# Performance work log

Measured on AMD Instinct MI355X. Metric: run time of the kernel, lower is better.

## Reference

```python
import jax, jax.numpy as jnp
import numpy as np

N = 65536      # nodes (256x256 grid)
E = 1048576    # edges (avg degree 16)
T_IN = 10      # TIME_STEPS_IN
L = 64         # LATENT_DIMS
MID = 128      # LATENT_DIMS * MLP_RATIO
GD = 2         # grid dims


def _lin_init(key, fan_in, fan_out):
    kw, kb = jax.random.split(key)
    s = 1.0 / np.sqrt(fan_in)
    W = jax.random.uniform(kw, (fan_in, fan_out), jnp.float32, -s, s)
    b = jax.random.uniform(kb, (fan_out,), jnp.float32, -s, s)
    return W, b


def setup_inputs() -> dict:
    key = jax.random.key(0)
    ks = jax.random.split(key, 10)
    x = jax.random.normal(ks[0], (N, T_IN), jnp.float32)
    grid = jax.random.uniform(ks[1], (N, GD), jnp.float32)
    edge_index = jax.random.randint(ks[2], (2, E), 0, N, jnp.int64)
    W_proj1, b_proj1 = _lin_init(ks[3], T_IN + GD, MID)
    W_proj2, b_proj2 = _lin_init(ks[4], MID, L)
    Wk, bk = _lin_init(ks[5], 2 * L + 2 * GD + 1, L)   # K edge MLP (single linear)
    Ww, bw = _lin_init(ks[6], L, L)                     # W node MLP (single linear)
    W_dec1, b_dec1 = _lin_init(ks[7], L, MID)
    W_dec2, b_dec2 = _lin_init(ks[8], MID, 1)
    return {"x": x, "grid": grid, "edge_index": edge_index,
            "W_proj1": W_proj1, "b_proj1": b_proj1, "W_proj2": W_proj2, "b_proj2": b_proj2,
            "Wk": Wk, "bk": bk, "Ww": Ww, "bw": bw,
            "W_dec1": W_dec1, "b_dec1": b_dec1, "W_dec2": W_dec2, "b_dec2": b_dec2}


def _gelu(x):
    return jax.nn.gelu(x, approximate=False)  # torch F.gelu default = exact erf


def reference(x, grid, edge_index, W_proj1, b_proj1, W_proj2, b_proj2,
              Wk, bk, Ww, bw, W_dec1, b_dec1, W_dec2, b_dec2):
    # project: cat(x, grid) -> Linear -> GELU -> Linear
    h = jnp.concatenate([x, grid], axis=-1)               # [N, T_IN+2]
    h = _gelu(h @ W_proj1 + b_proj1) @ W_proj2 + b_proj2  # [N, L]

    # message passing block (PyG source_to_target: j = row 0, i = row 1)
    src = edge_index[0]
    dst = edge_index[1]
    x_j = h[src]                                          # [E, L]
    x_i = h[dst]                                          # [E, L]
    g_j = grid[src]                                       # [E, 2]
    g_i = grid[dst]                                       # [E, 2]
    dist = jnp.sqrt(jnp.sum(jnp.square(g_i - g_j), axis=-1, keepdims=True))  # [E, 1]
    ef = jnp.concatenate([dist, g_i, g_j, x_i, x_j], axis=-1)  # [E, 2L+5]
    msg = ef @ Wk + bk                                    # [E, L]
    aggr = jax.ops.segment_sum(msg, dst, num_segments=N)  # [N, L]
    h = _gelu(h @ Ww + bw + aggr)                         # update

    # decode: Linear -> GELU -> Linear
    out = _gelu(h @ W_dec1 + b_dec1) @ W_dec2 + b_dec2    # [N, 1]
    return out
```

## Files before the change

kernel.cpp:

```cpp
#include <hip/hip_runtime.h>
#include <hip/hip_fp16.h>

static __device__ __forceinline__ float gelu(float x) {
    return 0.5f * x * (1.0f + erff(x * 0.70710678118654752f));
}

#define NBE 64
#define CAP 64

typedef _Float16 v8h __attribute__((ext_vector_type(8)));
typedef float    v4f __attribute__((ext_vector_type(4)));
union F8 { uint4 u; v8h v; _Float16 f[8]; };

static __device__ __forceinline__ void acc8(float* a, uint4 u) {
    float2 f0 = __half22float2(*(__half2*)&u.x);
    float2 f1 = __half22float2(*(__half2*)&u.y);
    float2 f2 = __half22float2(*(__half2*)&u.z);
    float2 f3 = __half22float2(*(__half2*)&u.w);
    a[0] += f0.x; a[1] += f0.y; a[2] += f1.x; a[3] += f1.y;
    a[4] += f2.x; a[5] += f2.y; a[6] += f3.x; a[7] += f3.y;
}

static __device__ __forceinline__ uint4 pack8(const float* v) {
    __half2 p0 = __floats2half2_rn(v[0], v[1]);
    __half2 p1 = __floats2half2_rn(v[2], v[3]);
    __half2 p2 = __floats2half2_rn(v[4], v[5]);
    __half2 p3 = __floats2half2_rn(v[6], v[7]);
    uint4 u;
    u.x = *(unsigned*)&p0; u.y = *(unsigned*)&p1;
    u.z = *(unsigned*)&p2; u.w = *(unsigned*)&p3;
    return u;
}

__global__ void __launch_bounds__(256, 1)
k_enc_scat(const float* __restrict__ x,
           const float* __restrict__ grid,
           const float* __restrict__ W1,
           const float* __restrict__ b1,
           const float* __restrict__ W2,
           const float* __restrict__ b2,
           const int* __restrict__ ei, int* __restrict__ cnt,
           int* __restrict__ ssrc,
           __half* __restrict__ h16, int N, int E, int encB)
{
    __shared__ float sx[NBE * 10];
    __shared__ float sg[NBE * 2];
    __shared__ float sm[NBE * 132];
    int tid = threadIdx.x;
    if ((int)blockIdx.x >= encB) {
        int e4 = (blockIdx.x - encB) * 256 + tid;
        if (e4 * 4 < E) {
            const int4* s4 = (const int4*)ei;
            const int4* d4 = (const int4*)(ei + E);
            int4 s = s4[e4];
            int4 d = d4[e4];
            int p;
            p = atomicAdd(&cnt[d.x], 1); if (p < CAP) ssrc[((size_t)d.x << 6) + p] = s.x;
            p = atomicAdd(&cnt[d.y], 1); if (p < CAP) ssrc[((size_t)d.y << 6) + p] = s.y;
            p = atomicAdd(&cnt[d.z], 1); if (p < CAP) ssrc[((size_t)d.z << 6) + p] = s.z;
            p = atomicAdd(&cnt[d.w], 1); if (p < CAP) ssrc[((size_t)d.w << 6) + p] = s.w;
        }
        return;
    }
    int n0 = blockIdx.x * NBE;
    for (int i = tid; i < NBE * 10; i += 256) sx[i] = x[(size_t)n0 * 10 + i];
    if (tid < NBE * 2) sg[tid] = grid[(size_t)n0 * 2 + tid];
    __syncthreads();

    int l = tid & 7, r = tid >> 3;
    int mb = 16 * l;
    float in[2][12];
#pragma unroll
    for (int m = 0; m < 2; m++) {
        int node = r + 32 * m;
#pragma unroll
        for (int k = 0; k < 10; k++) in[m][k] = sx[node * 10 + k];
        in[m][10] = sg[node * 2 + 0];
        in[m][11] = sg[node * 2 + 1];
    }

    float macc[2][16];
#pragma unroll
    for (int i = 0; i < 16; i++) {
        float b = b1[mb + i];
        macc[0][i] = b; macc[1][i] = b;
    }
#pragma unroll
    for (int k = 0; k < 12; k++) {
        const float4* w = (const float4*)(W1 + k * 128 + mb);
#pragma unroll
        for (int q = 0; q < 4; q++) {
            float4 wv = w[q];
#pragma unroll
            for (int m = 0; m < 2; m++) {
                float xv = in[m][k];
                macc[m][4 * q + 0] += xv * wv.x;
                macc[m][4 * q + 1] += xv * wv.y;
                macc[m][4 * q + 2] += xv * wv.z;
                macc[m][4 * q + 3] += xv * wv.w;
            }
        }
    }
#pragma unroll
    for (int m = 0; m < 2; m++) {
        float4* smp = (float4*)(sm + (r + 32 * m) * 132 + mb);
#pragma unroll
        for (int q = 0; q < 4; q++)
            smp[q] = make_float4(gelu(macc[m][4 * q]), gelu(macc[m][4 * q + 1]),
                                 gelu(macc[m][4 * q + 2]), gelu(macc[m][4 * q + 3]));
    }
    __syncthreads();

    int ob = 8 * l;
    float out8[2][8];
#pragma unroll
    for (int j = 0; j < 8; j++) {
        float b = b2[ob + j];
        out8[0][j] = b; out8[1][j] = b;
    }
#pragma unroll 2
    for (int i4 = 0; i4 < 128; i4 += 4) {
        float mva[2][4];
#pragma unroll
        for (int m = 0; m < 2; m++)
            *(float4*)mva[m] = *(const float4*)&sm[(r + 32 * m) * 132 + i4];
#pragma unroll
        for (int ii = 0; ii < 4; ii++) {
            const float4* w = (const float4*)(W2 + (i4 + ii) * 64 + ob);
            float4 w0 = w[0], w1 = w[1];
#pragma unroll
            for (int m = 0; m < 2; m++) {
                float mv = mva[m][ii];
                out8[m][0] += mv * w0.x; out8[m][1] += mv * w0.y;
                out8[m][2] += mv * w0.z; out8[m][3] += mv * w0.w;
                out8[m][4] += mv * w1.x; out8[m][5] += mv * w1.y;
                out8[m][6] += mv * w1.z; out8[m][7] += mv * w1.w;
            }
        }
    }
#pragma unroll
    for (int m = 0; m < 2; m++)
        ((uint4*)(h16 + (size_t)(n0 + r + 32 * m) * 64))[l] = pack8(out8[m]);
}

__global__ void k_gather(const __half* __restrict__ h16,
                         const float* __restrict__ grid,
                         const int* __restrict__ ssrc, const int* __restrict__ cnt,
                         __half* __restrict__ sum_h16, float* __restrict__ sum_g,
                         float* __restrict__ sum_d, int N)
{
    int tid = blockIdx.x * blockDim.x + threadIdx.x;
    int n = tid >> 3;
    int l = tid & 7;
    if (n >= N) return;
    int beg = n << 6;
    int dg = min(cnt[n], CAP);
    const uint4* h8 = (const uint4*)h16;
    float a0[8] = {0,0,0,0,0,0,0,0};
    float a1[8] = {0,0,0,0,0,0,0,0};
    float a2[8] = {0,0,0,0,0,0,0,0};
    float a3[8] = {0,0,0,0,0,0,0,0};
    float sgx = 0.f, sgy = 0.f, sd = 0.f, gix = 0.f, giy = 0.f;
    if (l == 0) { gix = grid[2 * n]; giy = grid[2 * n + 1]; }
    int i = 0;
    for (; i + 3 < dg; i += 4) {
        int4 s = *(const int4*)&ssrc[beg + i];
        uint4 u0 = h8[(size_t)s.x * 8 + l];
        uint4 u1 = h8[(size_t)s.y * 8 + l];
        uint4 u2 = h8[(size_t)s.z * 8 + l];
        uint4 u3 = h8[(size_t)s.w * 8 + l];
        acc8(a0, u0); acc8(a1, u1); acc8(a2, u2); acc8(a3, u3);
        if (l == 0) {
            float gx0 = grid[2 * s.x], gy0 = grid[2 * s.x + 1];
            float gx1 = grid[2 * s.y], gy1 = grid[2 * s.y + 1];
            float gx2 = grid[2 * s.z], gy2 = grid[2 * s.z + 1];
            float gx3 = grid[2 * s.w], gy3 = grid[2 * s.w + 1];
            float dx0 = gix - gx0, dy0 = giy - gy0;
            float dx1 = gix - gx1, dy1 = giy - gy1;
            float dx2 = gix - gx2, dy2 = giy - gy2;
            float dx3 = gix - gx3, dy3 = giy - gy3;
            sd += sqrtf(dx0 * dx0 + dy0 * dy0) + sqrtf(dx1 * dx1 + dy1 * dy1)
                + sqrtf(dx2 * dx2 + dy2 * dy2) + sqrtf(dx3 * dx3 + dy3 * dy3);
            sgx += gx0 + gx1 + gx2 + gx3;
            sgy += gy0 + gy1 + gy2 + gy3;
        }
    }
    for (; i < dg; i++) {
        int s0 = ssrc[beg + i];
        uint4 u0 = h8[(size_t)s0 * 8 + l];
        acc8(a0, u0);
        if (l == 0) {
            float gx0 = grid[2 * s0], gy0 = grid[2 * s0 + 1];
            float dx0 = gix - gx0, dy0 = giy - gy0;
            sd += sqrtf(dx0 * dx0 + dy0 * dy0);
            sgx += gx0; sgy += gy0;
        }
    }
#pragma unroll
    for (int j = 0; j < 8; j++) a0[j] += a1[j] + a2[j] + a3[j];
    ((uint4*)(sum_h16 + (size_t)n * 64))[l] = pack8(a0);
    if (l == 0) { sum_d[n] = sd; sum_g[2 * n] = sgx; sum_g[2 * n + 1] = sgy; }
}

__global__ void __launch_bounds__(256, 1)
k_update(const __half* __restrict__ h16, __half* __restrict__ sum_h16,
         const float* __restrict__ sum_g, const float* __restrict__ sum_d,
         const int* __restrict__ cnt, const float* __restrict__ grid,
         const float* __restrict__ Wk, const float* __restrict__ bk,
         const float* __restrict__ Ww, const float* __restrict__ bw, int N)
{
    __shared__ uint4 tabW[512];
    __shared__ uint4 tabC[512];
    __shared__ uint4 tabD[512];
    __shared__ uint4 tabV[256];
    int tid = threadIdx.x;

    for (int idx = tid; idx < 512; idx += 256) {
        int lane = idx & 63, nt = (idx >> 6) & 3, kc = idx >> 8;
        int col = nt * 16 + (lane & 15);
        int kr  = kc * 32 + ((lane >> 4) << 3);
        F8 fw, fc, fd;
#pragma unroll
        for (int j = 0; j < 8; j++) {
            fw.f[j] = (_Float16)Ww[(kr + j) * 64 + col];
            fc.f[j] = (_Float16)Wk[(size_t)(5 + kr + j) * 64 + col];
            fd.f[j] = (_Float16)Wk[(size_t)(69 + kr + j) * 64 + col];
        }
        tabW[idx] = fw.u; tabC[idx] = fc.u; tabD[idx] = fd.u;
    }
    if (tid < 256) {
        int lane = tid & 63, nt = tid >> 6;
        int col = nt * 16 + (lane & 15);
        F8 fv;
#pragma unroll
        for (int j = 0; j < 8; j++) fv.f[j] = (_Float16)0.f;
        if ((lane >> 4) == 0) {
            fv.f[0] = (_Float16)bw[col];
            fv.f[1] = (_Float16)bk[col];
            fv.f[2] = (_Float16)Wk[col];
            fv.f[3] = (_Float16)Wk[64 + col];
            fv.f[4] = (_Float16)Wk[128 + col];
            fv.f[5] = (_Float16)Wk[192 + col];
            fv.f[6] = (_Float16)Wk[256 + col];
        }
        tabV[tid] = fv.u;
    }
    __syncthreads();

    int lane = tid & 63, wave = tid >> 6;
    int m = lane & 15, quad = lane >> 4;
    const uint4* h8 = (const uint4*)h16;
    const uint4* s8 = (const uint4*)sum_h16;

    for (int t = 0; t < 2; t++) {
        int tile = blockIdx.x * 8 + wave * 2 + t;
        int base = tile * 16;
        int n = base + m;
        float deg = (float)cnt[n];
        float sd  = sum_d[n];
        float sgx = sum_g[2 * n], sgy = sum_g[2 * n + 1];
        float gix = grid[2 * n] * deg, giy = grid[2 * n + 1] * deg;

        F8 ah0, ah1, as0, as1, ahd0, ahd1, au;
        ah0.u = h8[(size_t)n * 8 + quad];
        ah1.u = h8[(size_t)n * 8 + 4 + quad];
        as0.u = s8[(size_t)n * 8 + quad];
        as1.u = s8[(size_t)n * 8 + 4 + quad];
        _Float16 dh = (_Float16)deg;
#pragma unroll
        for (int j = 0; j < 8; j++) { ahd0.f[j] = ah0.f[j] * dh; ahd1.f[j] = ah1.f[j] * dh; }
        float z = (quad == 0) ? 1.f : 0.f;
        au.f[0] = (_Float16)z;          au.f[1] = (_Float16)(deg * z);
        au.f[2] = (_Float16)(sd * z);   au.f[3] = (_Float16)(gix * z);
        au.f[4] = (_Float16)(giy * z);  au.f[5] = (_Float16)(sgx * z);
        au.f[6] = (_Float16)(sgy * z);  au.f[7] = (_Float16)0.f;

        float h2v[4][4];
#pragma unroll
        for (int nt = 0; nt < 4; nt++) {
            F8 bv, bw0, bw1, bc0, bc1, bd0, bd1f;
            bv.u  = tabV[nt * 64 + lane];
            bw0.u = tabW[nt * 64 + lane];       bw1.u = tabW[256 + nt * 64 + lane];
            bc0.u = tabC[nt * 64 + lane];       bc1.u = tabC[256 + nt * 64 + lane];
            bd0.u = tabD[nt * 64 + lane];       bd1f.u = tabD[256 + nt * 64 + lane];
            v4f acc = {0.f, 0.f, 0.f, 0.f};
            acc = __builtin_amdgcn_mfma_f32_16x16x32_f16(au.v,   bv.v,   acc, 0, 0, 0);
            acc = __builtin_amdgcn_mfma_f32_16x16x32_f16(ah0.v,  bw0.v,  acc, 0, 0, 0);
            acc = __builtin_amdgcn_mfma_f32_16x16x32_f16(ah1.v,  bw1.v,  acc, 0, 0, 0);
            acc = __builtin_amdgcn_mfma_f32_16x16x32_f16(ahd0.v, bc0.v,  acc, 0, 0, 0);
            acc = __builtin_amdgcn_mfma_f32_16x16x32_f16(ahd1.v, bc1.v,  acc, 0, 0, 0);
            acc = __builtin_amdgcn_mfma_f32_16x16x32_f16(as0.v,  bd0.v,  acc, 0, 0, 0);
            acc = __builtin_amdgcn_mfma_f32_16x16x32_f16(as1.v,  bd1f.v, acc, 0, 0, 0);
#pragma unroll
            for (int reg = 0; reg < 4; reg++) h2v[nt][reg] = gelu(acc[reg]);
        }
#pragma unroll
        for (int reg = 0; reg < 4; reg++) {
            int nr = base + quad * 4 + reg;
#pragma unroll
            for (int nt = 0; nt < 4; nt++)
                sum_h16[(size_t)nr * 64 + m + 16 * nt] = __float2half(h2v[nt][reg]);
        }
    }
}

__global__ void __launch_bounds__(256, 1)
k_decode(const __half* __restrict__ h2g,
         const float* __restrict__ Wd1, const float* __restrict__ bd1,
         const float* __restrict__ Wd2, const float* __restrict__ bd2,
         float* __restrict__ out, int N)
{
    __shared__ uint4 tab[1024];
    int tid = threadIdx.x;
    for (int idx = tid; idx < 1024; idx += 256) {
        int lane = idx & 63, nt = (idx >> 6) & 7, kc = idx >> 9;
        int col = nt * 16 + (lane & 15);
        int kr  = kc * 32 + ((lane >> 4) << 3);
        F8 f;
#pragma unroll
        for (int j = 0; j < 8; j++) f.f[j] = (_Float16)Wd1[(kr + j) * 128 + col];
        tab[idx] = f.u;
    }
    __syncthreads();

    int lane = tid & 63, wave = tid >> 6;
    int m = lane & 15, quad = lane >> 4;
    const uint4* h8 = (const uint4*)h2g;
    float bd2v = bd2[0];

    for (int t = 0; t < 2; t++) {
        int tile = blockIdx.x * 8 + wave * 2 + t;
        int base = tile * 16;
        int n = base + m;
        F8 ah0, ah1;
        ah0.u = h8[(size_t)n * 8 + quad];
        ah1.u = h8[(size_t)n * 8 + 4 + quad];
        float p[4] = {0.f, 0.f, 0.f, 0.f};
#pragma unroll
        for (int nt = 0; nt < 8; nt++) {
            int col = m + 16 * nt;
            float b = bd1[col];
            float w2 = Wd2[col];
            F8 b0, b1;
            b0.u = tab[nt * 64 + lane];
            b1.u = tab[512 + nt * 64 + lane];
            v4f acc = {b, b, b, b};
            acc = __builtin_amdgcn_mfma_f32_16x16x32_f16(ah0.v, b0.v, acc, 0, 0, 0);
            acc = __builtin_amdgcn_mfma_f32_16x16x32_f16(ah1.v, b1.v, acc, 0, 0, 0);
#pragma unroll
            for (int reg = 0; reg < 4; reg++) p[reg] += gelu(acc[reg]) * w2;
        }
#pragma unroll
        for (int reg = 0; reg < 4; reg++) {
            p[reg] += __shfl_xor(p[reg], 1);
            p[reg] += __shfl_xor(p[reg], 2);
            p[reg] += __shfl_xor(p[reg], 4);
            p[reg] += __shfl_xor(p[reg], 8);
        }
        if (m == 0) {
#pragma unroll
            for (int reg = 0; reg < 4; reg++)
                out[base + quad * 4 + reg] = p[reg] + bd2v;
        }
    }
}

extern "C" void kernel_launch(void* const* d_in, const int* in_sizes, int n_in,
                              void* d_out, int out_size, void* d_ws, size_t ws_size,
                              hipStream_t stream)
{
    const float* x    = (const float*)d_in[0];
    const float* grid = (const float*)d_in[1];
    const int*   ei   = (const int*)d_in[2];
    const float* W1   = (const float*)d_in[3];
    const float* b1   = (const float*)d_in[4];
    const float* W2   = (const float*)d_in[5];
    const float* b2   = (const float*)d_in[6];
    const float* Wk   = (const float*)d_in[7];
    const float* bk   = (const float*)d_in[8];
    const float* Ww   = (const float*)d_in[9];
    const float* bw   = (const float*)d_in[10];
    const float* Wd1  = (const float*)d_in[11];
    const float* bd1  = (const float*)d_in[12];
    const float* Wd2  = (const float*)d_in[13];
    const float* bd2  = (const float*)d_in[14];
    float* out = (float*)d_out;

    int N = in_sizes[0] / 10;
    int E = in_sizes[2] / 2;

    char* ws = (char*)d_ws;
    size_t o_h16  = 0;
    size_t o_sh16 = o_h16  + (size_t)N * 64 * 2;
    size_t o_sumg = o_sh16 + (size_t)N * 64 * 2;
    size_t o_sumd = o_sumg + (size_t)N * 2 * 4;
    size_t o_cnt  = o_sumd + (size_t)N * 4;
    size_t o_ssrc = o_cnt  + (size_t)N * 4;

    __half* h16     = (__half*)(ws + o_h16);
    __half* sum_h16 = (__half*)(ws + o_sh16);
    float* sum_g = (float*)(ws + o_sumg);
    float* sum_d = (float*)(ws + o_sumd);
    int*   cnt   = (int*)  (ws + o_cnt);
    int*   ssrc  = (int*)  (ws + o_ssrc);

    hipMemsetAsync(cnt, 0, (size_t)N * 4, stream);

    int encB  = N / NBE;
    int scatB = (E / 4 + 255) / 256;
    k_enc_scat<<<dim3(encB + scatB), dim3(256), 0, stream>>>(x, grid, W1, b1, W2, b2,
                                                             ei, cnt, ssrc, h16, N, E, encB);
    k_gather<<<dim3((N * 8 + 255) / 256), dim3(256), 0, stream>>>(h16, grid, ssrc, cnt,
                                                                   sum_h16, sum_g, sum_d, N);
    int tiles = N / 16;
    k_update<<<dim3(tiles / 8), dim3(256), 0, stream>>>(h16, sum_h16, sum_g, sum_d, cnt,
                                                        grid, Wk, bk, Ww, bw, N);
    k_decode<<<dim3(tiles / 8), dim3(256), 0, stream>>>(sum_h16, Wd1, bd1, Wd2, bd2, out, N);
}
```

Baseline: 235.4 us.

## Store edge source indices as 16-bit, parallelize grid gather, shrink encoder tile

Edge source indices in the CSR-like bucket are stored as unsigned short, which halves the scatter writes and the gather index reads. The gather kernel spreads the per-edge grid loads and distance math across four lanes and combines them with xor shuffles instead of serializing on lane 0. The encoder now processes 32 nodes per block and keeps the hidden activations in fp16 shared memory, with one node per thread group. The 16-bit indices only hold for N up to 65536, and the fp16 intermediate adds rounding.

After: 284.1 us. +20.7%, slower.

```diff
diff --git a/kernel.cpp b/kernel.cpp
--- a/kernel.cpp
+++ b/kernel.cpp
@@ -5,7 +5,8 @@
     return 0.5f * x * (1.0f + erff(x * 0.70710678118654752f));
 }
 
-#define NBE 64
+#define NBE 32
+#define SM  136
 #define CAP 64
 
 typedef _Float16 v8h __attribute__((ext_vector_type(8)));
@@ -40,12 +41,12 @@
            const float* __restrict__ W2,
            const float* __restrict__ b2,
            const int* __restrict__ ei, int* __restrict__ cnt,
-           int* __restrict__ ssrc,
+           unsigned short* __restrict__ ssrc,
            __half* __restrict__ h16, int N, int E, int encB)
 {
     __shared__ float sx[NBE * 10];
     __shared__ float sg[NBE * 2];
-    __shared__ float sm[NBE * 132];
+    __shared__ __half sm[NBE * SM];
     int tid = threadIdx.x;
     if ((int)blockIdx.x >= encB) {
         int e4 = (blockIdx.x - encB) * 256 + tid;
@@ -55,10 +56,10 @@
             int4 s = s4[e4];
             int4 d = d4[e4];
             int p;
-            p = atomicAdd(&cnt[d.x], 1); if (p < CAP) ssrc[((size_t)d.x << 6) + p] = s.x;
-            p = atomicAdd(&cnt[d.y], 1); if (p < CAP) ssrc[((size_t)d.y << 6) + p] = s.y;
-            p = atomicAdd(&cnt[d.z], 1); if (p < CAP) ssrc[((size_t)d.z << 6) + p] = s.z;
-            p = atomicAdd(&cnt[d.w], 1); if (p < CAP) ssrc[((size_t)d.w << 6) + p] = s.w;
+            p = atomicAdd(&cnt[d.x], 1); if (p < CAP) ssrc[((size_t)d.x << 6) + p] = (unsigned short)s.x;
+            p = atomicAdd(&cnt[d.y], 1); if (p < CAP) ssrc[((size_t)d.y << 6) + p] = (unsigned short)s.y;
+            p = atomicAdd(&cnt[d.z], 1); if (p < CAP) ssrc[((size_t)d.z << 6) + p] = (unsigned short)s.z;
+            p = atomicAdd(&cnt[d.w], 1); if (p < CAP) ssrc[((size_t)d.w << 6) + p] = (unsigned short)s.w;
         }
         return;
     }
@@ -67,85 +68,71 @@
     if (tid < NBE * 2) sg[tid] = grid[(size_t)n0 * 2 + tid];
     __syncthreads();
 
-    int l = tid & 7, r = tid >> 3;
+    int l = tid & 7, nl = tid >> 3;
     int mb = 16 * l;
-    float in[2][12];
-#pragma unroll
-    for (int m = 0; m < 2; m++) {
-        int node = r + 32 * m;
-#pragma unroll
-        for (int k = 0; k < 10; k++) in[m][k] = sx[node * 10 + k];
-        in[m][10] = sg[node * 2 + 0];
-        in[m][11] = sg[node * 2 + 1];
-    }
-
-    float macc[2][16];
-#pragma unroll
-    for (int i = 0; i < 16; i++) {
-        float b = b1[mb + i];
-        macc[0][i] = b; macc[1][i] = b;
-    }
+    float in[12];
+#pragma unroll
+    for (int k = 0; k < 10; k++) in[k] = sx[nl * 10 + k];
+    in[10] = sg[nl * 2 + 0];
+    in[11] = sg[nl * 2 + 1];
+
+    float macc[16];
+#pragma unroll
+    for (int i = 0; i < 16; i++) macc[i] = b1[mb + i];
 #pragma unroll
     for (int k = 0; k < 12; k++) {
+        float xv = in[k];
         const float4* w = (const float4*)(W1 + k * 128 + mb);
 #pragma unroll
         for (int q = 0; q < 4; q++) {
             float4 wv = w[q];
-#pragma unroll
-            for (int m = 0; m < 2; m++) {
-                float xv = in[m][k];
-                macc[m][4 * q + 0] += xv * wv.x;
-                macc[m][4 * q + 1] += xv * wv.y;
-                macc[m][4 * q + 2] += xv * wv.z;
-                macc[m][4 * q + 3] += xv * wv.w;
-            }
-        }
-    }
-#pragma unroll
-    for (int m = 0; m < 2; m++) {
-        float4* smp = (float4*)(sm + (r + 32 * m) * 132 + mb);
-#pragma unroll
-        for (int q = 0; q < 4; q++)
-            smp[q] = make_float4(gelu(macc[m][4 * q]), gelu(macc[m][4 * q + 1]),
-                                 gelu(macc[m][4 * q + 2]), gelu(macc[m][4 * q + 3]));
-    }
+            macc[4 * q + 0] += xv * wv.x;
+            macc[4 * q + 1] += xv * wv.y;
+            macc[4 * q + 2] += xv * wv.z;
+            macc[4 * q + 3] += xv * wv.w;
+        }
+    }
+    float g16[16];
+#pragma unroll
+    for (int i = 0; i < 16; i++) g16[i] = gelu(macc[i]);
+    *(uint4*)&sm[nl * SM + mb]     = pack8(g16);
+    *(uint4*)&sm[nl * SM + mb + 8] = pack8(g16 + 8);
     __syncthreads();
 
     int ob = 8 * l;
-    float out8[2][8];
-#pragma unroll
-    for (int j = 0; j < 8; j++) {
-        float b = b2[ob + j];
-        out8[0][j] = b; out8[1][j] = b;
-    }
+    float out8[8];
+#pragma unroll
+    for (int j = 0; j < 8; j++) out8[j] = b2[ob + j];
+    const __half* smn = sm + nl * SM;
 #pragma unroll 2
-    for (int i4 = 0; i4 < 128; i4 += 4) {
-        float mva[2][4];
-#pragma unroll
-        for (int m = 0; m < 2; m++)
-            *(float4*)mva[m] = *(const float4*)&sm[(r + 32 * m) * 132 + i4];
-#pragma unroll
-        for (int ii = 0; ii < 4; ii++) {
-            const float4* w = (const float4*)(W2 + (i4 + ii) * 64 + ob);
+    for (int i8 = 0; i8 < 128; i8 += 8) {
+        F8 mu;
+        mu.u = *(const uint4*)&smn[i8];
+        float mv[8];
+        float2 t0 = __half22float2(*(__half2*)&mu.u.x);
+        float2 t1 = __half22float2(*(__half2*)&mu.u.y);
+        float2 t2 = __half22float2(*(__half2*)&mu.u.z);
+        float2 t3 = __half22float2(*(__half2*)&mu.u.w);
+        mv[0] = t0.x; mv[1] = t0.y; mv[2] = t1.x; mv[3] = t1.y;
+        mv[4] = t2.x; mv[5] = t2.y; mv[6] = t3.x; mv[7] = t3.y;
+#pragma unroll
+        for (int ii = 0; ii < 8; ii++) {
+            const float4* w = (const float4*)(W2 + (i8 + ii) * 64 + ob);
             float4 w0 = w[0], w1 = w[1];
-#pragma unroll
-            for (int m = 0; m < 2; m++) {
-                float mv = mva[m][ii];
-                out8[m][0] += mv * w0.x; out8[m][1] += mv * w0.y;
-                out8[m][2] += mv * w0.z; out8[m][3] += mv * w0.w;
-                out8[m][4] += mv * w1.x; out8[m][5] += mv * w1.y;
-                out8[m][6] += mv * w1.z; out8[m][7] += mv * w1.w;
-            }
-        }
-    }
-#pragma unroll
-    for (int m = 0; m < 2; m++)
-        ((uint4*)(h16 + (size_t)(n0 + r + 32 * m) * 64))[l] = pack8(out8[m]);
+            float m = mv[ii];
+            out8[0] += m * w0.x; out8[1] += m * w0.y;
+            out8[2] += m * w0.z; out8[3] += m * w0.w;
+            out8[4] += m * w1.x; out8[5] += m * w1.y;
+            out8[6] += m * w1.z; out8[7] += m * w1.w;
+        }
+    }
+    ((uint4*)(h16 + (size_t)(n0 + nl) * 64))[l] = pack8(out8);
 }
 
 __global__ void k_gather(const __half* __restrict__ h16,
                          const float* __restrict__ grid,
-                         const int* __restrict__ ssrc, const int* __restrict__ cnt,
+                         const unsigned short* __restrict__ ssrc,
+                         const int* __restrict__ cnt,
                          __half* __restrict__ sum_h16, float* __restrict__ sum_g,
                          float* __restrict__ sum_d, int N)
 {
@@ -153,51 +140,49 @@
     int n = tid >> 3;
     int l = tid & 7;
     if (n >= N) return;
-    int beg = n << 6;
+    const unsigned short* ss = ssrc + ((size_t)n << 6);
     int dg = min(cnt[n], CAP);
     const uint4* h8 = (const uint4*)h16;
     float a0[8] = {0,0,0,0,0,0,0,0};
     float a1[8] = {0,0,0,0,0,0,0,0};
     float a2[8] = {0,0,0,0,0,0,0,0};
     float a3[8] = {0,0,0,0,0,0,0,0};
-    float sgx = 0.f, sgy = 0.f, sd = 0.f, gix = 0.f, giy = 0.f;
-    if (l == 0) { gix = grid[2 * n]; giy = grid[2 * n + 1]; }
+    float sgx = 0.f, sgy = 0.f, sd = 0.f;
+    float gix = grid[2 * n], giy = grid[2 * n + 1];
     int i = 0;
     for (; i + 3 < dg; i += 4) {
-        int4 s = *(const int4*)&ssrc[beg + i];
-        uint4 u0 = h8[(size_t)s.x * 8 + l];
-        uint4 u1 = h8[(size_t)s.y * 8 + l];
-        uint4 u2 = h8[(size_t)s.z * 8 + l];
-        uint4 u3 = h8[(size_t)s.w * 8 + l];
+        uint2 sv = *(const uint2*)&ss[i];
+        int s0 = sv.x & 0xffff, s1 = sv.x >> 16;
+        int s2 = sv.y & 0xffff, s3 = sv.y >> 16;
+        uint4 u0 = h8[(size_t)s0 * 8 + l];
+        uint4 u1 = h8[(size_t)s1 * 8 + l];
+        uint4 u2 = h8[(size_t)s2 * 8 + l];
+        uint4 u3 = h8[(size_t)s3 * 8 + l];
         acc8(a0, u0); acc8(a1, u1); acc8(a2, u2); acc8(a3, u3);
-        if (l == 0) {
-            float gx0 = grid[2 * s.x], gy0 = grid[2 * s.x + 1];
-            float gx1 = grid[2 * s.y], gy1 = grid[2 * s.y + 1];
-            float gx2 = grid[2 * s.z], gy2 = grid[2 * s.z + 1];
-            float gx3 = grid[2 * s.w], gy3 = grid[2 * s.w + 1];
-            float dx0 = gix - gx0, dy0 = giy - gy0;
-            float dx1 = gix - gx1, dy1 = giy - gy1;
-            float dx2 = gix - gx2, dy2 = giy - gy2;
-            float dx3 = gix - gx3, dy3 = giy - gy3;
-            sd += sqrtf(dx0 * dx0 + dy0 * dy0) + sqrtf(dx1 * dx1 + dy1 * dy1)
-                + sqrtf(dx2 * dx2 + dy2 * dy2) + sqrtf(dx3 * dx3 + dy3 * dy3);
-            sgx += gx0 + gx1 + gx2 + gx3;
-            sgy += gy0 + gy1 + gy2 + gy3;
+        if (l < 4) {
+            int sj = (l == 0) ? s0 : (l == 1) ? s1 : (l == 2) ? s2 : s3;
+            float2 g = *(const float2*)&grid[2 * sj];
+            float dx = gix - g.x, dy = giy - g.y;
+            sd += sqrtf(dx * dx + dy * dy);
+            sgx += g.x; sgy += g.y;
         }
     }
     for (; i < dg; i++) {
-        int s0 = ssrc[beg + i];
+        int s0 = ss[i];
         uint4 u0 = h8[(size_t)s0 * 8 + l];
         acc8(a0, u0);
         if (l == 0) {
-            float gx0 = grid[2 * s0], gy0 = grid[2 * s0 + 1];
-            float dx0 = gix - gx0, dy0 = giy - gy0;
-            sd += sqrtf(dx0 * dx0 + dy0 * dy0);
-            sgx += gx0; sgy += gy0;
+            float2 g = *(const float2*)&grid[2 * s0];
+            float dx = gix - g.x, dy = giy - g.y;
+            sd += sqrtf(dx * dx + dy * dy);
+            sgx += g.x; sgy += g.y;
         }
     }
 #pragma unroll
     for (int j = 0; j < 8; j++) a0[j] += a1[j] + a2[j] + a3[j];
+    sd  += __shfl_xor(sd, 1);  sd  += __shfl_xor(sd, 2);  sd  += __shfl_xor(sd, 4);
+    sgx += __shfl_xor(sgx, 1); sgx += __shfl_xor(sgx, 2); sgx += __shfl_xor(sgx, 4);
+    sgy += __shfl_xor(sgy, 1); sgy += __shfl_xor(sgy, 2); sgy += __shfl_xor(sgy, 4);
     ((uint4*)(sum_h16 + (size_t)n * 64))[l] = pack8(a0);
     if (l == 0) { sum_d[n] = sd; sum_g[2 * n] = sgx; sum_g[2 * n + 1] = sgy; }
 }
@@ -402,7 +387,7 @@
     float* sum_g = (float*)(ws + o_sumg);
     float* sum_d = (float*)(ws + o_sumd);
     int*   cnt   = (int*)  (ws + o_cnt);
-    int*   ssrc  = (int*)  (ws + o_ssrc);
+    unsigned short* ssrc = (unsigned short*)(ws + o_ssrc);
 
     hipMemsetAsync(cnt, 0, (size_t)N * 4, stream);
 
```
